# Kernel optimization log

Measured on AMD Instinct MI355X. Metric: run time of the kernel, lower is better.

The kernel has to match this reference:

```python
import jax, jax.numpy as jnp
import numpy as np

EMBED = 256; M = 8; DV = 32; L = 4; K = 4; SCALE = 0.5
LEVELS = [(128, 128), (64, 64), (32, 32), (16, 16)]  # (H_l, W_l), static
S_TOTAL = sum(h * w for h, w in LEVELS)  # 21760


def _linear_params(key, fan_in, fan_out):
    kw, kb = jax.random.split(key)
    lim = 1.0 / np.sqrt(fan_in)
    W = jax.random.uniform(kw, (fan_in, fan_out), minval=-lim, maxval=lim, dtype=jnp.float32)
    b = jax.random.uniform(kb, (fan_out,), minval=-lim, maxval=lim, dtype=jnp.float32)
    return W, b


def setup_inputs() -> dict:
    key = jax.random.key(0)
    ks = jax.random.split(key, 8)
    N, Q = 2, 8192
    W_off, b_off = _linear_params(ks[0], EMBED, M * L * K * 2)
    W_attn, b_attn = _linear_params(ks[1], EMBED, M * L * K)
    W_val, b_val = _linear_params(ks[2], EMBED, M * DV)
    W_out, b_out = _linear_params(ks[3], M * DV, EMBED)
    queries = jax.random.normal(ks[4], (N, Q, EMBED), dtype=jnp.float32)
    query_geometry_logits = jax.random.normal(ks[5], (N, Q, 4), dtype=jnp.float32)
    value = jax.random.normal(ks[6], (N, S_TOTAL, EMBED), dtype=jnp.float32)
    value_mask = jnp.ones((N, S_TOTAL, 1), dtype=jnp.float32)
    return {"queries": queries, "query_geometry_logits": query_geometry_logits,
            "value": value, "value_mask": value_mask,
            "W_off": W_off, "b_off": b_off, "W_attn": W_attn, "b_attn": b_attn,
            "W_val": W_val, "b_val": b_val, "W_out": W_out, "b_out": b_out}


def _bilinear(img_flat, grid, H, W):
    """grid_sample(mode=bilinear, padding=zeros, align_corners=False).
    img_flat: (B, H*W, C); grid: (B, P, 2) with (x, y) in [-1, 1]."""
    x = (grid[..., 0] + 1.0) * (W * 0.5) - 0.5
    y = (grid[..., 1] + 1.0) * (H * 0.5) - 0.5
    x0f, y0f = jnp.floor(x), jnp.floor(y)
    wx, wy = x - x0f, y - y0f
    x0, y0 = x0f.astype(jnp.int32), y0f.astype(jnp.int32)

    def gather(xi, yi, w):
        valid = (xi >= 0) & (xi < W) & (yi >= 0) & (yi < H)
        idx = jnp.clip(yi, 0, H - 1) * W + jnp.clip(xi, 0, W - 1)
        v = jnp.take_along_axis(img_flat, idx[..., None], axis=1)
        return v * (w * valid)[..., None]

    return (gather(x0, y0, (1 - wx) * (1 - wy)) + gather(x0 + 1, y0, wx * (1 - wy))
            + gather(x0, y0 + 1, (1 - wx) * wy) + gather(x0 + 1, y0 + 1, wx * wy))


def _forward(queries, query_geometry_logits, value, value_mask,
             W_off, b_off, W_attn, b_attn, W_val, b_val, W_out, b_out):
    N, Q, _ = queries.shape
    # attention weights: (N, Q, M, L*K), softmax over the L*K sampling points
    attn = jax.nn.softmax((queries @ W_attn + b_attn).reshape(N, Q, M, L * K), axis=-1)
    # sampling offsets: (N, Q, M, L*K, 2)
    deltas = (queries @ W_off + b_off).reshape(N, Q, M, L * K, 2)
    # reference boxes: sigmoid -> (cx, cy, w, h) in [0, 1]
    b_q = jax.nn.sigmoid(query_geometry_logits)
    xy, wh = b_q[..., :2], b_q[..., 2:]
    scale = wh * (1.0 / K) * SCALE                       # (N, Q, 2)
    pos = xy[:, :, None, None, :] + deltas * scale[:, :, None, None, :]  # (N,Q,M,LK,2)
    # value projection + mask
    v_masked = value_mask * (value @ W_val + b_val)      # (N, S, M*DV)
    # collapse (N, M) for per-head grid sampling
    grid = jnp.clip(2.0 * pos.transpose(0, 2, 1, 3, 4).reshape(N * M, Q, L * K, 2) - 1.0, -1.0, 1.0)
    outs, start = [], 0
    for li, (H, W) in enumerate(LEVELS):
        v_l = v_masked[:, start:start + H * W, :].reshape(N, H * W, M, DV)
        v_l = v_l.transpose(0, 2, 1, 3).reshape(N * M, H * W, DV)
        g_l = grid[:, :, K * li:K * (li + 1), :].reshape(N * M, Q * K, 2)
        s_l = _bilinear(v_l, g_l, H, W)                  # (N*M, Q*K, DV)
        outs.append(s_l.reshape(N, M, Q, K, DV))
        start += H * W
    vals = jnp.concatenate(outs, axis=3)                 # (N, M, Q, L*K, DV)
    vals = vals.transpose(0, 2, 1, 3, 4)                 # (N, Q, M, L*K, DV)
    out = jnp.sum(attn[..., None] * vals, axis=3).reshape(N, Q, M * DV)
    return out @ W_out + b_out                           # (N, Q, EMBED)


def reference(queries, query_geometry_logits, value, value_mask,
              W_off, b_off, W_attn, b_attn, W_val, b_val, W_out, b_out):
    return _forward(queries, query_geometry_logits, value, value_mask,
                    W_off, b_off, W_attn, b_attn, W_val, b_val, W_out, b_out)
```

## Files before the change

### kernel.cpp

```cpp
#include <hip/hip_runtime.h>
#include <math.h>

#define EMBED   256
#define M_HEADS 8
#define DVAL    32
#define LK      16
#define S_TOTAL 21760
#define NQ      8192
#define NROWS   (2 * NQ)
#define QBS     16

typedef __attribute__((ext_vector_type(8))) short s16x8;
typedef __attribute__((ext_vector_type(4))) float f32x4;
typedef unsigned short u16;
typedef unsigned int   u32;

__device__ __forceinline__ short f2bf(float f) {
    unsigned u = __float_as_uint(f);
    u += 0x7fffu + ((u >> 16) & 1u);
    return (short)(u >> 16);
}
__device__ __forceinline__ float bf2f(short h) {
    return __uint_as_float(((unsigned)(u16)h) << 16);
}

#define V_OFF     0
#define V_FLTS    5570560
#define PA_OFF    (V_OFF + V_FLTS)
#define PA_FLTS   6291456
#define MID_OFF   (PA_OFF + PA_FLTS)
#define MID_FLTS  2097152
#define WHI_OFF   (MID_OFF + MID_FLTS)
#define WOA_FLTS  49152
#define WLO_OFF   (WHI_OFF + WOA_FLTS)
#define WV_OFF    (WLO_OFF + WOA_FLTS)
#define WO_OFF    (WV_OFF + 32768)

__global__ __launch_bounds__(256) void prep_kernel(
    const float* __restrict__ W_off, const float* __restrict__ W_attn,
    u16* __restrict__ Whi,           u16* __restrict__ Wlo,
    const float* __restrict__ W_val, u16* __restrict__ Wv,
    const float* __restrict__ W_out, u16* __restrict__ Wo)
{
    const int b = blockIdx.x;
    const int t = threadIdx.x;

    if (b < 512) {
        const int flat = b * 256 + t;
        const int which = flat >> 16;
        const int e = flat & 65535;
        const int k = e >> 8, c = e & 255;
        const float f = which ? W_out[k * 256 + c] : W_val[k * 256 + c];
        const int kt = k >> 5, qd = (k >> 3) & 3, j = k & 7;
        const int idx = (((kt * 256 + c) << 2) + qd) * 8 + j;
        (which ? Wo : Wv)[idx] = (u16)f2bf(f);
    } else {
        const int flat = (b - 512) * 256 + t;
        const int k = flat / 384, c = flat - k * 384;
        const float f = (c < 256) ? W_off[k * 256 + c] : W_attn[k * 128 + (c - 256)];
        const short h = f2bf(f);
        const short lo = f2bf(f - bf2f(h));
        const int kt = k >> 5, qd = (k >> 3) & 3, j = k & 7;
        const int idx = (((kt * 384 + c) << 2) + qd) * 8 + j;
        Whi[idx] = (u16)h;
        Wlo[idx] = (u16)lo;
    }
}

__global__ __launch_bounds__(256, 2) void vproj_kernel(
    const float* __restrict__ value,
    const float* __restrict__ vmask,
    const u16* __restrict__ Wpk,
    const float* __restrict__ b_val,
    u16* __restrict__ v_out)
{
    const int t  = threadIdx.x;
    const int w  = t >> 6, l = t & 63;
    const int c  = l & 15, qd = l >> 4;
    const int c0 = w * 64;

    s16x8 B[8][4];
    #pragma unroll
    for (int kt = 0; kt < 8; ++kt)
        #pragma unroll
        for (int nt = 0; nt < 4; ++nt)
            B[kt][nt] = *(const s16x8*)(Wpk + (((kt * 256 + c0 + nt * 16 + c) << 2) + qd) * 8);

    float bias[4];
    #pragma unroll
    for (int nt = 0; nt < 4; ++nt) bias[nt] = b_val[c0 + nt * 16 + c];

    for (int tile = blockIdx.x; tile < 2720; tile += 512) {
        const int r0 = tile * 16;
        const float* __restrict__ ap = value + (size_t)(r0 + c) * EMBED + qd * 8;

        float4 a0[8], a1[8];
        #pragma unroll
        for (int kt = 0; kt < 8; ++kt) {
            a0[kt] = *(const float4*)(ap + kt * 32);
            a1[kt] = *(const float4*)(ap + kt * 32 + 4);
        }

        f32x4 acc[4] = {};
        #pragma unroll
        for (int kt = 0; kt < 8; ++kt) {
            const s16x8 a = (s16x8){ f2bf(a0[kt].x), f2bf(a0[kt].y), f2bf(a0[kt].z), f2bf(a0[kt].w),
                                     f2bf(a1[kt].x), f2bf(a1[kt].y), f2bf(a1[kt].z), f2bf(a1[kt].w) };
            #pragma unroll
            for (int nt = 0; nt < 4; ++nt)
                acc[nt] = __builtin_amdgcn_mfma_f32_16x16x32_bf16(a, B[kt][nt], acc[nt], 0, 0, 0);
        }

        #pragma unroll
        for (int r = 0; r < 4; ++r) {
            const int grow = r0 + qd * 4 + r;
            const int n = (grow >= S_TOTAL) ? 1 : 0;
            const int s = grow - n * S_TOTAL;
            const float mk = vmask[grow];
            #pragma unroll
            for (int nt = 0; nt < 4; ++nt) {
                const int col = c0 + nt * 16 + c;
                const int hm = col >> 5, d = col & 31;
                v_out[((size_t)(n * M_HEADS + hm) * S_TOTAL + s) * DVAL + d] =
                    (u16)f2bf((acc[nt][r] + bias[nt]) * mk);
            }
        }
    }
}

__global__ __launch_bounds__(256) void qproj_kernel(
    const float* __restrict__ queries,
    const float* __restrict__ qgl,
    const u16* __restrict__ Whi, const u16* __restrict__ Wlo,
    const float* __restrict__ b_off, const float* __restrict__ b_attn,
    float* __restrict__ pa)
{
    __shared__ float s_off[32][260];
    __shared__ float s_attn[32][132];
    __shared__ float s_geom[32][4];

    const int t  = threadIdx.x;
    const int w  = t >> 6, l = t & 63;
    const int c  = l & 15, qd = l >> 4;
    const int row0 = blockIdx.x * 32;
    const int c0 = w * 96;

    if (t < 32) {
        const float* g = &qgl[(size_t)(row0 + t) * 4];
        s_geom[t][0] = 1.f / (1.f + __expf(-g[0]));
        s_geom[t][1] = 1.f / (1.f + __expf(-g[1]));
        s_geom[t][2] = (1.f / (1.f + __expf(-g[2]))) * 0.125f;
        s_geom[t][3] = (1.f / (1.f + __expf(-g[3]))) * 0.125f;
    }

    f32x4 acc[2][6] = {};

    for (int kt = 0; kt < 8; ++kt) {
        s16x8 ah[2], al[2], bh[6], bl[6];
        #pragma unroll
        for (int mt = 0; mt < 2; ++mt) {
            const float* qp = queries + (size_t)(row0 + mt * 16 + c) * EMBED + kt * 32 + qd * 8;
            const float4 v0 = *(const float4*)qp;
            const float4 v1 = *(const float4*)(qp + 4);
            const short h0 = f2bf(v0.x), h1 = f2bf(v0.y), h2 = f2bf(v0.z), h3 = f2bf(v0.w);
            const short h4 = f2bf(v1.x), h5 = f2bf(v1.y), h6 = f2bf(v1.z), h7 = f2bf(v1.w);
            ah[mt] = (s16x8){ h0, h1, h2, h3, h4, h5, h6, h7 };
            al[mt] = (s16x8){ f2bf(v0.x - bf2f(h0)), f2bf(v0.y - bf2f(h1)),
                              f2bf(v0.z - bf2f(h2)), f2bf(v0.w - bf2f(h3)),
                              f2bf(v1.x - bf2f(h4)), f2bf(v1.y - bf2f(h5)),
                              f2bf(v1.z - bf2f(h6)), f2bf(v1.w - bf2f(h7)) };
        }
        #pragma unroll
        for (int nt = 0; nt < 6; ++nt) {
            const int idx = (((kt * 384 + c0 + nt * 16 + c) << 2) + qd) * 8;
            bh[nt] = *(const s16x8*)(Whi + idx);
            bl[nt] = *(const s16x8*)(Wlo + idx);
        }
        #pragma unroll
        for (int mt = 0; mt < 2; ++mt)
            #pragma unroll
            for (int nt = 0; nt < 6; ++nt) {
                acc[mt][nt] = __builtin_amdgcn_mfma_f32_16x16x32_bf16(ah[mt], bh[nt], acc[mt][nt], 0, 0, 0);
                acc[mt][nt] = __builtin_amdgcn_mfma_f32_16x16x32_bf16(ah[mt], bl[nt], acc[mt][nt], 0, 0, 0);
                acc[mt][nt] = __builtin_amdgcn_mfma_f32_16x16x32_bf16(al[mt], bh[nt], acc[mt][nt], 0, 0, 0);
            }
    }

    #pragma unroll
    for (int mt = 0; mt < 2; ++mt)
        #pragma unroll
        for (int nt = 0; nt < 6; ++nt) {
            const int col = c0 + nt * 16 + c;
            #pragma unroll
            for (int r = 0; r < 4; ++r) {
                const int row = mt * 16 + qd * 4 + r;
                if (col < 256) s_off[row][col] = acc[mt][nt][r] + b_off[col];
                else           s_attn[row][col - 256] = acc[mt][nt][r] + b_attn[col - 256];
            }
        }
    __syncthreads();

    {
        const int qi = t >> 3, hm = t & 7;
        float* a = &s_attn[qi][hm * LK];
        float mx = a[0];
        #pragma unroll
        for (int i = 1; i < LK; ++i) mx = fmaxf(mx, a[i]);
        float s = 0.f;
        #pragma unroll
        for (int i = 0; i < LK; ++i) { const float e = __expf(a[i] - mx); a[i] = e; s += e; }
        const float inv = 1.f / s;
        #pragma unroll
        for (int i = 0; i < LK; ++i) a[i] *= inv;
    }
    __syncthreads();

    for (int p = t; p < 32 * 128; p += 256) {
        const int qi = p >> 7;
        const int pt = p & 127;
        const int lvl = (pt & 15) >> 2;
        const float Wl = (float)(128 >> lvl);
        const float px = fmaf(s_off[qi][2 * pt + 0], s_geom[qi][2], s_geom[qi][0]);
        const float py = fmaf(s_off[qi][2 * pt + 1], s_geom[qi][3], s_geom[qi][1]);
        const float gx = fminf(fmaxf(2.f * px - 1.f, -1.f), 1.f);
        const float gy = fminf(fmaxf(2.f * py - 1.f, -1.f), 1.f);
        const float x = (gx + 1.f) * (Wl * 0.5f) - 0.5f;
        const float y = (gy + 1.f) * (Wl * 0.5f) - 0.5f;
        const size_t idx = ((size_t)(row0 + qi) * 128 + pt) * 3;
        pa[idx + 0] = x;
        pa[idx + 1] = y;
        pa[idx + 2] = s_attn[qi][pt];
    }
}

__global__ __launch_bounds__(256) void sample_kernel(
    const float* __restrict__ pa,
    const u16* __restrict__ v_tab,
    u16* __restrict__ mid)
{
    __shared__ int4   s_idx[QBS * 17];
    __shared__ float4 s_w[QBS * 17];

    const int t    = threadIdx.x;
    const int m    = blockIdx.x & 7;
    const int rest = blockIdx.x >> 3;
    const int qc   = rest & 511;
    const int n    = rest >> 9;
    const int q0   = qc * QBS;

    {
        const int qi = t >> 4, lk = t & 15;
        const int lvl   = lk >> 2;
        const int Wl    = 128 >> lvl;
        const int start = (lvl == 0) ? 0 : (lvl == 1) ? 16384 : (lvl == 2) ? 20480 : 21504;

        const size_t prow = ((size_t)(n * NQ + q0 + qi)) * 128 + m * 16 + lk;
        const float x  = pa[prow * 3 + 0];
        const float y  = pa[prow * 3 + 1];
        const float aw = pa[prow * 3 + 2];

        const float x0f = floorf(x), y0f = floorf(y);
        const int   x0 = (int)x0f, y0 = (int)y0f;
        const float wx = x - x0f, wy = y - y0f;

        const float vx0 = (x0 >= 0) ? 1.f : 0.f;
        const float vx1 = (x0 + 1 <= Wl - 1) ? 1.f : 0.f;
        const float vy0 = (y0 >= 0) ? 1.f : 0.f;
        const float vy1 = (y0 + 1 <= Wl - 1) ? 1.f : 0.f;

        const int xc0 = max(x0, 0);
        const int xc1 = min(x0 + 1, Wl - 1);
        const int yc0 = max(y0, 0);
        const int yc1 = min(y0 + 1, Wl - 1);

        const int e = qi * 17 + lk;
        s_idx[e] = make_int4((start + yc0 * Wl + xc0) * DVAL,
                             (start + yc0 * Wl + xc1) * DVAL,
                             (start + yc1 * Wl + xc0) * DVAL,
                             (start + yc1 * Wl + xc1) * DVAL);
        s_w[e] = make_float4(aw * (1.f - wx) * (1.f - wy) * vx0 * vy0,
                             aw * wx * (1.f - wy) * vx1 * vy0,
                             aw * (1.f - wx) * wy * vx0 * vy1,
                             aw * wx * wy * vx1 * vy1);
    }
    __syncthreads();

    const int g = t >> 4, dp = t & 15;
    const u16* __restrict__ vbp =
        v_tab + (size_t)(n * M_HEADS + m) * S_TOTAL * DVAL + 2 * dp;

    float acc0 = 0.f, acc1 = 0.f;
    #pragma unroll
    for (int lk = 0; lk < LK; ++lk) {
        const int4   id = s_idx[g * 17 + lk];
        const float4 w  = s_w[g * 17 + lk];
        const u32 u0 = *(const u32*)(vbp + id.x);
        const u32 u1 = *(const u32*)(vbp + id.y);
        const u32 u2 = *(const u32*)(vbp + id.z);
        const u32 u3 = *(const u32*)(vbp + id.w);
        acc0 = fmaf(w.x, __uint_as_float(u0 << 16), acc0);
        acc1 = fmaf(w.x, __uint_as_float(u0 & 0xffff0000u), acc1);
        acc0 = fmaf(w.y, __uint_as_float(u1 << 16), acc0);
        acc1 = fmaf(w.y, __uint_as_float(u1 & 0xffff0000u), acc1);
        acc0 = fmaf(w.z, __uint_as_float(u2 << 16), acc0);
        acc1 = fmaf(w.z, __uint_as_float(u2 & 0xffff0000u), acc1);
        acc0 = fmaf(w.w, __uint_as_float(u3 << 16), acc0);
        acc1 = fmaf(w.w, __uint_as_float(u3 & 0xffff0000u), acc1);
    }

    const u32 packed = ((u32)(u16)f2bf(acc1) << 16) | (u32)(u16)f2bf(acc0);
    *(u32*)(mid + ((size_t)(n * NQ + q0 + g)) * EMBED + m * DVAL + 2 * dp) = packed;
}

__global__ __launch_bounds__(256, 2) void out_kernel(
    const u16* __restrict__ mid,
    const u16* __restrict__ Wpk,
    const float* __restrict__ b_out,
    float* __restrict__ out)
{
    const int t  = threadIdx.x;
    const int w  = t >> 6, l = t & 63;
    const int c  = l & 15, qd = l >> 4;
    const int c0 = w * 64;

    s16x8 B[8][4];
    #pragma unroll
    for (int kt = 0; kt < 8; ++kt)
        #pragma unroll
        for (int nt = 0; nt < 4; ++nt)
            B[kt][nt] = *(const s16x8*)(Wpk + (((kt * 256 + c0 + nt * 16 + c) << 2) + qd) * 8);

    float bias[4];
    #pragma unroll
    for (int nt = 0; nt < 4; ++nt) bias[nt] = b_out[c0 + nt * 16 + c];

    for (int tile = blockIdx.x; tile < 1024; tile += 512) {
        const int r0 = tile * 16;
        const u16* __restrict__ ap = mid + (size_t)(r0 + c) * EMBED + qd * 8;

        s16x8 a[8];
        #pragma unroll
        for (int kt = 0; kt < 8; ++kt)
            a[kt] = *(const s16x8*)(ap + kt * 32);

        f32x4 acc[4] = {};
        #pragma unroll
        for (int kt = 0; kt < 8; ++kt)
            #pragma unroll
            for (int nt = 0; nt < 4; ++nt)
                acc[nt] = __builtin_amdgcn_mfma_f32_16x16x32_bf16(a[kt], B[kt][nt], acc[nt], 0, 0, 0);

        #pragma unroll
        for (int r = 0; r < 4; ++r) {
            const int row = r0 + qd * 4 + r;
            #pragma unroll
            for (int nt = 0; nt < 4; ++nt)
                out[(size_t)row * EMBED + c0 + nt * 16 + c] = acc[nt][r] + bias[nt];
        }
    }
}

extern "C" void kernel_launch(void* const* d_in, const int* in_sizes, int n_in,
                              void* d_out, int out_size, void* d_ws, size_t ws_size,
                              hipStream_t stream) {
    (void)in_sizes; (void)n_in; (void)out_size; (void)ws_size;

    const float* queries = (const float*)d_in[0];
    const float* qgl     = (const float*)d_in[1];
    const float* value   = (const float*)d_in[2];
    const float* vmask   = (const float*)d_in[3];
    const float* W_off   = (const float*)d_in[4];
    const float* b_off   = (const float*)d_in[5];
    const float* W_attn  = (const float*)d_in[6];
    const float* b_attn  = (const float*)d_in[7];
    const float* W_val   = (const float*)d_in[8];
    const float* b_val   = (const float*)d_in[9];
    const float* W_out   = (const float*)d_in[10];
    const float* b_out   = (const float*)d_in[11];

    float* ws   = (float*)d_ws;
    u16*  v_ws  = (u16*)(ws + V_OFF);
    float* pa   = ws + PA_OFF;
    u16*  mid   = (u16*)(ws + MID_OFF);
    u16*  whi   = (u16*)(ws + WHI_OFF);
    u16*  wlo   = (u16*)(ws + WLO_OFF);
    u16*  wvpk  = (u16*)(ws + WV_OFF);
    u16*  wopk  = (u16*)(ws + WO_OFF);
    float* outp = (float*)d_out;

    prep_kernel<<<896, 256, 0, stream>>>(W_off, W_attn, whi, wlo,
                                         W_val, wvpk, W_out, wopk);

    vproj_kernel<<<512, 256, 0, stream>>>(value, vmask, wvpk, b_val, v_ws);
    qproj_kernel<<<NROWS / 32, 256, 0, stream>>>(queries, qgl, whi, wlo,
                                                 b_off, b_attn, pa);
    sample_kernel<<<2 * (NQ / QBS) * M_HEADS, 256, 0, stream>>>(pa, v_ws, mid);
    out_kernel<<<512, 256, 0, stream>>>(mid, wopk, b_out, outp);
}
```

Before: 205.1 us.

## Merge value and query projections into one launch; widen sampler per-thread vectors

Fuses the value-projection and query-projection kernels into a single launch whose block index chooses the branch, so the two independent GEMMs can run concurrently and one launch is saved. The sampling kernel now handles 32 queries per block, with each thread gathering 4 bf16 channels (uint2) instead of 2. This halves the thread count per output and doubles the bytes per gather. The fused kernel inherits the launch_bounds(256,2) and the larger register footprint of the vproj path, which may constrain the qproj branch's occupancy.

```diff
diff --git a/kernel.cpp b/kernel.cpp
--- a/kernel.cpp
+++ b/kernel.cpp
@@ -8,7 +8,7 @@
 #define S_TOTAL 21760
 #define NQ      8192
 #define NROWS   (2 * NQ)
-#define QBS     16
+#define QBS     32
 
 typedef __attribute__((ext_vector_type(8))) short s16x8;
 typedef __attribute__((ext_vector_type(4))) float f32x4;
@@ -67,68 +67,12 @@
     }
 }
 
-__global__ __launch_bounds__(256, 2) void vproj_kernel(
+__global__ __launch_bounds__(256, 2) void stage1_kernel(
     const float* __restrict__ value,
     const float* __restrict__ vmask,
     const u16* __restrict__ Wpk,
     const float* __restrict__ b_val,
-    u16* __restrict__ v_out)
-{
-    const int t  = threadIdx.x;
-    const int w  = t >> 6, l = t & 63;
-    const int c  = l & 15, qd = l >> 4;
-    const int c0 = w * 64;
-
-    s16x8 B[8][4];
-    #pragma unroll
-    for (int kt = 0; kt < 8; ++kt)
-        #pragma unroll
-        for (int nt = 0; nt < 4; ++nt)
-            B[kt][nt] = *(const s16x8*)(Wpk + (((kt * 256 + c0 + nt * 16 + c) << 2) + qd) * 8);
-
-    float bias[4];
-    #pragma unroll
-    for (int nt = 0; nt < 4; ++nt) bias[nt] = b_val[c0 + nt * 16 + c];
-
-    for (int tile = blockIdx.x; tile < 2720; tile += 512) {
-        const int r0 = tile * 16;
-        const float* __restrict__ ap = value + (size_t)(r0 + c) * EMBED + qd * 8;
-
-        float4 a0[8], a1[8];
-        #pragma unroll
-        for (int kt = 0; kt < 8; ++kt) {
-            a0[kt] = *(const float4*)(ap + kt * 32);
-            a1[kt] = *(const float4*)(ap + kt * 32 + 4);
-        }
-
-        f32x4 acc[4] = {};
-        #pragma unroll
-        for (int kt = 0; kt < 8; ++kt) {
-            const s16x8 a = (s16x8){ f2bf(a0[kt].x), f2bf(a0[kt].y), f2bf(a0[kt].z), f2bf(a0[kt].w),
-                                     f2bf(a1[kt].x), f2bf(a1[kt].y), f2bf(a1[kt].z), f2bf(a1[kt].w) };
-            #pragma unroll
-            for (int nt = 0; nt < 4; ++nt)
-                acc[nt] = __builtin_amdgcn_mfma_f32_16x16x32_bf16(a, B[kt][nt], acc[nt], 0, 0, 0);
-        }
-
-        #pragma unroll
-        for (int r = 0; r < 4; ++r) {
-            const int grow = r0 + qd * 4 + r;
-            const int n = (grow >= S_TOTAL) ? 1 : 0;
-            const int s = grow - n * S_TOTAL;
-            const float mk = vmask[grow];
-            #pragma unroll
-            for (int nt = 0; nt < 4; ++nt) {
-                const int col = c0 + nt * 16 + c;
-                const int hm = col >> 5, d = col & 31;
-                v_out[((size_t)(n * M_HEADS + hm) * S_TOTAL + s) * DVAL + d] =
-                    (u16)f2bf((acc[nt][r] + bias[nt]) * mk);
-            }
-        }
-    }
-}
-
-__global__ __launch_bounds__(256) void qproj_kernel(
+    u16* __restrict__ v_out,
     const float* __restrict__ queries,
     const float* __restrict__ qgl,
     const u16* __restrict__ Whi, const u16* __restrict__ Wlo,
@@ -142,7 +86,61 @@
     const int t  = threadIdx.x;
     const int w  = t >> 6, l = t & 63;
     const int c  = l & 15, qd = l >> 4;
-    const int row0 = blockIdx.x * 32;
+
+    if (blockIdx.x < 512) {
+        const int c0 = w * 64;
+
+        s16x8 B[8][4];
+        #pragma unroll
+        for (int kt = 0; kt < 8; ++kt)
+            #pragma unroll
+            for (int nt = 0; nt < 4; ++nt)
+                B[kt][nt] = *(const s16x8*)(Wpk + (((kt * 256 + c0 + nt * 16 + c) << 2) + qd) * 8);
+
+        float bias[4];
+        #pragma unroll
+        for (int nt = 0; nt < 4; ++nt) bias[nt] = b_val[c0 + nt * 16 + c];
+
+        for (int tile = blockIdx.x; tile < 2720; tile += 512) {
+            const int r0 = tile * 16;
+            const float* __restrict__ ap = value + (size_t)(r0 + c) * EMBED + qd * 8;
+
+            float4 a0[8], a1[8];
+            #pragma unroll
+            for (int kt = 0; kt < 8; ++kt) {
+                a0[kt] = *(const float4*)(ap + kt * 32);
+                a1[kt] = *(const float4*)(ap + kt * 32 + 4);
+            }
+
+            f32x4 acc[4] = {};
+            #pragma unroll
+            for (int kt = 0; kt < 8; ++kt) {
+                const s16x8 a = (s16x8){ f2bf(a0[kt].x), f2bf(a0[kt].y), f2bf(a0[kt].z), f2bf(a0[kt].w),
+                                         f2bf(a1[kt].x), f2bf(a1[kt].y), f2bf(a1[kt].z), f2bf(a1[kt].w) };
+                #pragma unroll
+                for (int nt = 0; nt < 4; ++nt)
+                    acc[nt] = __builtin_amdgcn_mfma_f32_16x16x32_bf16(a, B[kt][nt], acc[nt], 0, 0, 0);
+            }
+
+            #pragma unroll
+            for (int r = 0; r < 4; ++r) {
+                const int grow = r0 + qd * 4 + r;
+                const int n = (grow >= S_TOTAL) ? 1 : 0;
+                const int s = grow - n * S_TOTAL;
+                const float mk = vmask[grow];
+                #pragma unroll
+                for (int nt = 0; nt < 4; ++nt) {
+                    const int col = c0 + nt * 16 + c;
+                    const int hm = col >> 5, d = col & 31;
+                    v_out[((size_t)(n * M_HEADS + hm) * S_TOTAL + s) * DVAL + d] =
+                        (u16)f2bf((acc[nt][r] + bias[nt]) * mk);
+                }
+            }
+        }
+        return;
+    }
+
+    const int row0 = (blockIdx.x - 512) * 32;
     const int c0 = w * 96;
 
     if (t < 32) {
@@ -238,18 +236,20 @@
     const u16* __restrict__ v_tab,
     u16* __restrict__ mid)
 {
-    __shared__ int4   s_idx[QBS * 17];
-    __shared__ float4 s_w[QBS * 17];
+    __shared__ int4   s_idx[QBS * LK];
+    __shared__ float4 s_w[QBS * LK];
 
     const int t    = threadIdx.x;
     const int m    = blockIdx.x & 7;
     const int rest = blockIdx.x >> 3;
-    const int qc   = rest & 511;
-    const int n    = rest >> 9;
+    const int qc   = rest & 255;
+    const int n    = rest >> 8;
     const int q0   = qc * QBS;
 
-    {
-        const int qi = t >> 4, lk = t & 15;
+    #pragma unroll
+    for (int pp = 0; pp < 2; ++pp) {
+        const int e  = t + pp * 256;
+        const int qi = e >> 4, lk = e & 15;
         const int lvl   = lk >> 2;
         const int Wl    = 128 >> lvl;
         const int start = (lvl == 0) ? 0 : (lvl == 1) ? 16384 : (lvl == 2) ? 20480 : 21504;
@@ -273,7 +273,6 @@
         const int yc0 = max(y0, 0);
         const int yc1 = min(y0 + 1, Wl - 1);
 
-        const int e = qi * 17 + lk;
         s_idx[e] = make_int4((start + yc0 * Wl + xc0) * DVAL,
                              (start + yc0 * Wl + xc1) * DVAL,
                              (start + yc1 * Wl + xc0) * DVAL,
@@ -285,31 +284,41 @@
     }
     __syncthreads();
 
-    const int g = t >> 4, dp = t & 15;
+    const int g = t >> 3, dp = t & 7;
     const u16* __restrict__ vbp =
-        v_tab + (size_t)(n * M_HEADS + m) * S_TOTAL * DVAL + 2 * dp;
-
-    float acc0 = 0.f, acc1 = 0.f;
+        v_tab + (size_t)(n * M_HEADS + m) * S_TOTAL * DVAL + 4 * dp;
+
+    float acc0 = 0.f, acc1 = 0.f, acc2 = 0.f, acc3 = 0.f;
     #pragma unroll
     for (int lk = 0; lk < LK; ++lk) {
-        const int4   id = s_idx[g * 17 + lk];
-        const float4 w  = s_w[g * 17 + lk];
-        const u32 u0 = *(const u32*)(vbp + id.x);
-        const u32 u1 = *(const u32*)(vbp + id.y);
-        const u32 u2 = *(const u32*)(vbp + id.z);
-        const u32 u3 = *(const u32*)(vbp + id.w);
-        acc0 = fmaf(w.x, __uint_as_float(u0 << 16), acc0);
-        acc1 = fmaf(w.x, __uint_as_float(u0 & 0xffff0000u), acc1);
-        acc0 = fmaf(w.y, __uint_as_float(u1 << 16), acc0);
-        acc1 = fmaf(w.y, __uint_as_float(u1 & 0xffff0000u), acc1);
-        acc0 = fmaf(w.z, __uint_as_float(u2 << 16), acc0);
-        acc1 = fmaf(w.z, __uint_as_float(u2 & 0xffff0000u), acc1);
-        acc0 = fmaf(w.w, __uint_as_float(u3 << 16), acc0);
-        acc1 = fmaf(w.w, __uint_as_float(u3 & 0xffff0000u), acc1);
-    }
-
-    const u32 packed = ((u32)(u16)f2bf(acc1) << 16) | (u32)(u16)f2bf(acc0);
-    *(u32*)(mid + ((size_t)(n * NQ + q0 + g)) * EMBED + m * DVAL + 2 * dp) = packed;
+        const int4   id = s_idx[g * LK + lk];
+        const float4 w  = s_w[g * LK + lk];
+        const uint2 u0 = *(const uint2*)(vbp + id.x);
+        const uint2 u1 = *(const uint2*)(vbp + id.y);
+        const uint2 u2 = *(const uint2*)(vbp + id.z);
+        const uint2 u3 = *(const uint2*)(vbp + id.w);
+        acc0 = fmaf(w.x, __uint_as_float(u0.x << 16), acc0);
+        acc1 = fmaf(w.x, __uint_as_float(u0.x & 0xffff0000u), acc1);
+        acc2 = fmaf(w.x, __uint_as_float(u0.y << 16), acc2);
+        acc3 = fmaf(w.x, __uint_as_float(u0.y & 0xffff0000u), acc3);
+        acc0 = fmaf(w.y, __uint_as_float(u1.x << 16), acc0);
+        acc1 = fmaf(w.y, __uint_as_float(u1.x & 0xffff0000u), acc1);
+        acc2 = fmaf(w.y, __uint_as_float(u1.y << 16), acc2);
+        acc3 = fmaf(w.y, __uint_as_float(u1.y & 0xffff0000u), acc3);
+        acc0 = fmaf(w.z, __uint_as_float(u2.x << 16), acc0);
+        acc1 = fmaf(w.z, __uint_as_float(u2.x & 0xffff0000u), acc1);
+        acc2 = fmaf(w.z, __uint_as_float(u2.y << 16), acc2);
+        acc3 = fmaf(w.z, __uint_as_float(u2.y & 0xffff0000u), acc3);
+        acc0 = fmaf(w.w, __uint_as_float(u3.x << 16), acc0);
+        acc1 = fmaf(w.w, __uint_as_float(u3.x & 0xffff0000u), acc1);
+        acc2 = fmaf(w.w, __uint_as_float(u3.y << 16), acc2);
+        acc3 = fmaf(w.w, __uint_as_float(u3.y & 0xffff0000u), acc3);
+    }
+
+    uint2 packed;
+    packed.x = ((u32)(u16)f2bf(acc1) << 16) | (u32)(u16)f2bf(acc0);
+    packed.y = ((u32)(u16)f2bf(acc3) << 16) | (u32)(u16)f2bf(acc2);
+    *(uint2*)(mid + ((size_t)(n * NQ + q0 + g)) * EMBED + m * DVAL + 4 * dp) = packed;
 }
 
 __global__ __launch_bounds__(256, 2) void out_kernel(
@@ -391,9 +400,9 @@
     prep_kernel<<<896, 256, 0, stream>>>(W_off, W_attn, whi, wlo,
                                          W_val, wvpk, W_out, wopk);
 
-    vproj_kernel<<<512, 256, 0, stream>>>(value, vmask, wvpk, b_val, v_ws);
-    qproj_kernel<<<NROWS / 32, 256, 0, stream>>>(queries, qgl, whi, wlo,
-                                                 b_off, b_attn, pa);
+    stage1_kernel<<<1024, 256, 0, stream>>>(value, vmask, wvpk, b_val, v_ws,
+                                            queries, qgl, whi, wlo,
+                                            b_off, b_attn, pa);
     sample_kernel<<<2 * (NQ / QBS) * M_HEADS, 256, 0, stream>>>(pa, v_ws, mid);
     out_kernel<<<512, 256, 0, stream>>>(mid, wopk, b_out, outp);
 }
```

After: 212.4 us. 3.6% more time.
